# Performance work log

Hardware: AMD Instinct MI355X
Metric: run time of the kernel (lower is better)

## Reference

```python
import jax, jax.numpy as jnp
import numpy as np

B, S_IMG, S_TXT, D, H, HD = 1, 4096, 512, 3072, 24, 128
EPS = 1e-5
SCALE = 1.0 / np.sqrt(HD)


def _linear(x, W, b=None):
    # torch nn.Linear: y = x @ W.T + b, W is [out, in]
    y = jnp.einsum('bsd,od->bso', x, W)
    return y if b is None else y + b


def _rmsnorm(x, w):
    # over last dim (head_dim), torch nn.RMSNorm with affine weight
    var = jnp.mean(jnp.square(x), axis=-1, keepdims=True)
    return x * jax.lax.rsqrt(var + EPS) * w


def _rope(x, cos, sin):
    # x: [B, S, H, D]; cos/sin: [S, D]; interleaved-pair rotation
    xr = x.reshape(*x.shape[:-1], HD // 2, 2)
    x_real, x_imag = xr[..., 0], xr[..., 1]
    x_rot = jnp.stack([-x_imag, x_real], axis=-1).reshape(x.shape)
    return x * cos[None, :, None, :] + x_rot * sin[None, :, None, :]


def setup_inputs() -> dict:
    key = jax.random.key(0)
    ks = jax.random.split(key, 24)
    s = 0.02
    inp = {
        'hidden_states': jax.random.normal(ks[0], (B, S_IMG, D), jnp.float32),
        'encoder_hidden_states': jax.random.normal(ks[1], (B, S_TXT, D), jnp.float32),
        'rope_cos': jax.random.uniform(ks[2], (S_IMG + S_TXT, HD), jnp.float32),
        'rope_sin': jax.random.uniform(ks[3], (S_IMG + S_TXT, HD), jnp.float32),
        # image-stream qkv (bias=False)
        'Wq': jax.random.normal(ks[4], (D, D), jnp.float32) * s,
        'Wk': jax.random.normal(ks[5], (D, D), jnp.float32) * s,
        'Wv': jax.random.normal(ks[6], (D, D), jnp.float32) * s,
        # text-stream qkv (bias=True)
        'Waq': jax.random.normal(ks[7], (D, D), jnp.float32) * s,
        'baq': jnp.zeros((D,), jnp.float32),
        'Wak': jax.random.normal(ks[8], (D, D), jnp.float32) * s,
        'bak': jnp.zeros((D,), jnp.float32),
        'Wav': jax.random.normal(ks[9], (D, D), jnp.float32) * s,
        'bav': jnp.zeros((D,), jnp.float32),
        # output projections (bias=True)
        'Wo': jax.random.normal(ks[10], (D, D), jnp.float32) * s,
        'bo': jnp.zeros((D,), jnp.float32),
        'Wao': jax.random.normal(ks[11], (D, D), jnp.float32) * s,
        'bao': jnp.zeros((D,), jnp.float32),
        # RMSNorm weights on head_dim
        'wq_norm': jnp.ones((HD,), jnp.float32),
        'wk_norm': jnp.ones((HD,), jnp.float32),
        'waq_norm': jnp.ones((HD,), jnp.float32),
        'wak_norm': jnp.ones((HD,), jnp.float32),
    }
    return inp


def reference(hidden_states, encoder_hidden_states, rope_cos, rope_sin,
              Wq, Wk, Wv, Waq, baq, Wak, bak, Wav, bav,
              Wo, bo, Wao, bao, wq_norm, wk_norm, waq_norm, wak_norm):
    # image-stream qkv -> [B, S_img, H, HD]
    q = _linear(hidden_states, Wq).reshape(B, S_IMG, H, HD)
    k = _linear(hidden_states, Wk).reshape(B, S_IMG, H, HD)
    v = _linear(hidden_states, Wv).reshape(B, S_IMG, H, HD)
    q = _rmsnorm(q, wq_norm)
    k = _rmsnorm(k, wk_norm)
    # text-stream qkv -> [B, S_txt, H, HD]
    eq = _linear(encoder_hidden_states, Waq, baq).reshape(B, S_TXT, H, HD)
    ek = _linear(encoder_hidden_states, Wak, bak).reshape(B, S_TXT, H, HD)
    ev = _linear(encoder_hidden_states, Wav, bav).reshape(B, S_TXT, H, HD)
    eq = _rmsnorm(eq, waq_norm)
    ek = _rmsnorm(ek, wak_norm)
    # concat [encoder, image] along sequence
    q = jnp.concatenate([eq, q], axis=1)  # [B, S_total, H, HD]
    k = jnp.concatenate([ek, k], axis=1)
    v = jnp.concatenate([ev, v], axis=1)
    # RoPE on joint sequence
    q = _rope(q, rope_cos, rope_sin)
    k = _rope(k, rope_cos, rope_sin)
    # SDPA over joint sequence
    scores = jnp.einsum('bqhd,bkhd->bhqk', q, k) * SCALE
    probs = jax.nn.softmax(scores, axis=-1)
    out = jnp.einsum('bhqk,bkhd->bqhd', probs, v)  # [B, S_total, H, HD]
    out = out.reshape(B, S_IMG + S_TXT, D)
    enc_out = _linear(out[:, :S_TXT], Wao, bao)
    img_out = _linear(out[:, S_TXT:], Wo, bo)
    return (img_out, enc_out)
```

## Files before the change

### kernel.cpp

```cpp
#include <hip/hip_runtime.h>

typedef __bf16 bf16_t;
typedef __bf16 bf16x8 __attribute__((ext_vector_type(8)));
typedef float  f32x4  __attribute__((ext_vector_type(4)));

#define S_IMG 4096
#define S_TXT 512
#define S_TOT 4608
#define DMODEL 3072
#define NH 24
#define HD 128

__device__ __forceinline__ void load_lds16(const void* g, void* l) {
  __builtin_amdgcn_global_load_lds(
      (const __attribute__((address_space(1))) void*)g,
      (__attribute__((address_space(3))) void*)l, 16, 0, 0);
}

#define BARRIER() do { asm volatile("" ::: "memory");                          \
                       __builtin_amdgcn_s_barrier();                           \
                       asm volatile("" ::: "memory"); } while (0)

__global__ __launch_bounds__(256) void f2b_kernel(const float* __restrict__ in,
                                                  bf16_t* __restrict__ out, int n) {
  int i = (blockIdx.x * 256 + threadIdx.x) * 4;
  if (i >= n) return;
  float4 v = *(const float4*)(in + i);
  union { bf16_t b[4]; uint2 u; } pk;
  pk.b[0] = (bf16_t)v.x; pk.b[1] = (bf16_t)v.y;
  pk.b[2] = (bf16_t)v.z; pk.b[3] = (bf16_t)v.w;
  *(uint2*)(out + i) = pk.u;
}

template <typename OT>
__global__ __launch_bounds__(512, 2) void gemm256(
    const bf16_t* __restrict__ A0, const bf16_t* __restrict__ B0,
    OT* __restrict__ C0, const float* __restrict__ bias0, int mt0,
    const bf16_t* __restrict__ A1, const bf16_t* __restrict__ B1,
    OT* __restrict__ C1, const float* __restrict__ bias1, int swzq)
{
  const int NT = DMODEL / 64;
  __shared__ bf16_t As[2][2][256 * 32];
  __shared__ bf16_t Bs[2][2][256 * 32];

  int bid = blockIdx.x;
  int t = (bid & 7) * swzq + (bid >> 3);
  int nb0 = mt0 * 12;
  const bf16_t* A; const bf16_t* B; OT* C; const float* bias;
  if (t < nb0) { A = A0; B = B0; C = C0; bias = bias0; }
  else { t -= nb0; A = A1; B = B1; C = C1; bias = bias1; }
  int bx = t % 12, by = t / 12;

  int tid = threadIdx.x;
  int lane = tid & 63, wid = tid >> 6;
  int l15 = lane & 15, lg = lane >> 4;
  int wm = wid >> 2, wn = wid & 3;

  const bf16_t* Ag = A + (size_t)by * 256 * DMODEL;
  const bf16_t* Bg = B + (size_t)bx * 256 * DMODEL;

  int ur0 = tid >> 2;
  int uc0 = (tid & 3) * 8;

  auto stage = [&](int ht) {
    int T = ht >> 2, sl = ht & 3, kh = sl >> 1;
    const bf16_t* G = (sl & 1) ? Bg : Ag;
    bf16_t* L = (sl & 1) ? &Bs[T & 1][kh][0] : &As[T & 1][kh][0];
    int kbase = T * 64 + kh * 32;
    #pragma unroll
    for (int j = 0; j < 2; j++) {
      int r = j * 128 + ur0;
      load_lds16(G + (size_t)r * DMODEL + kbase + uc0,
                 (char*)L + (size_t)(j * 512 + tid) * 16);
    }
  };

  f32x4 acc[8][4];
  f32x4 zero = {0.f, 0.f, 0.f, 0.f};
  #pragma unroll
  for (int m = 0; m < 8; m++)
    #pragma unroll
    for (int n = 0; n < 4; n++) acc[m][n] = zero;

  stage(0); stage(1); stage(2); stage(3); stage(4); stage(5);
  asm volatile("s_waitcnt vmcnt(8)" ::: "memory");
  BARRIER();

  for (int T = 0; T < NT; ++T) {
    int cur = T & 1;
    const bf16_t* A0s = &As[cur][0][0];
    const bf16_t* A1s = &As[cur][1][0];
    const bf16_t* B0s = &Bs[cur][0][0];
    const bf16_t* B1s = &Bs[cur][1][0];
    bf16x8 af[4], bfr[4];

    #pragma unroll
    for (int n = 0; n < 4; n++)
      bfr[n] = *(const bf16x8*)(B0s + (wn * 64 + n * 16 + l15) * 32 + lg * 8);
    #pragma unroll
    for (int m = 0; m < 4; m++)
      af[m] = *(const bf16x8*)(A0s + (wm * 128 + m * 16 + l15) * 32 + lg * 8);
    if (T + 1 < NT) stage(4 * T + 6);
    BARRIER();
    __builtin_amdgcn_s_setprio(1);
    #pragma unroll
    for (int m = 0; m < 4; m++)
      #pragma unroll
      for (int n = 0; n < 4; n++)
        acc[m][n] = __builtin_amdgcn_mfma_f32_16x16x32_bf16(af[m], bfr[n], acc[m][n], 0, 0, 0);
    __builtin_amdgcn_s_setprio(0);
    BARRIER();

    #pragma unroll
    for (int m = 0; m < 4; m++)
      af[m] = *(const bf16x8*)(A0s + (wm * 128 + 64 + m * 16 + l15) * 32 + lg * 8);
    if (T + 1 < NT) stage(4 * T + 7);
    BARRIER();
    __builtin_amdgcn_s_setprio(1);
    #pragma unroll
    for (int m = 0; m < 4; m++)
      #pragma unroll
      for (int n = 0; n < 4; n++)
        acc[4 + m][n] = __builtin_amdgcn_mfma_f32_16x16x32_bf16(af[m], bfr[n], acc[4 + m][n], 0, 0, 0);
    __builtin_amdgcn_s_setprio(0);
    if (T < NT - 1) asm volatile("s_waitcnt vmcnt(8)" ::: "memory");
    else            asm volatile("s_waitcnt vmcnt(0)" ::: "memory");
    BARRIER();

    #pragma unroll
    for (int n = 0; n < 4; n++)
      bfr[n] = *(const bf16x8*)(B1s + (wn * 64 + n * 16 + l15) * 32 + lg * 8);
    #pragma unroll
    for (int m = 0; m < 4; m++)
      af[m] = *(const bf16x8*)(A1s + (wm * 128 + m * 16 + l15) * 32 + lg * 8);
    if (T + 2 < NT) stage(4 * T + 8);
    BARRIER();
    __builtin_amdgcn_s_setprio(1);
    #pragma unroll
    for (int m = 0; m < 4; m++)
      #pragma unroll
      for (int n = 0; n < 4; n++)
        acc[m][n] = __builtin_amdgcn_mfma_f32_16x16x32_bf16(af[m], bfr[n], acc[m][n], 0, 0, 0);
    __builtin_amdgcn_s_setprio(0);
    BARRIER();

    #pragma unroll
    for (int m = 0; m < 4; m++)
      af[m] = *(const bf16x8*)(A1s + (wm * 128 + 64 + m * 16 + l15) * 32 + lg * 8);
    if (T + 2 < NT) stage(4 * T + 9);
    BARRIER();
    __builtin_amdgcn_s_setprio(1);
    #pragma unroll
    for (int m = 0; m < 4; m++)
      #pragma unroll
      for (int n = 0; n < 4; n++)
        acc[4 + m][n] = __builtin_amdgcn_mfma_f32_16x16x32_bf16(af[m], bfr[n], acc[4 + m][n], 0, 0, 0);
    __builtin_amdgcn_s_setprio(0);
    if (T < NT - 2)      asm volatile("s_waitcnt vmcnt(8)" ::: "memory");
    else if (T == NT - 2) asm volatile("s_waitcnt vmcnt(4)" ::: "memory");
    BARRIER();
  }

  size_t row0 = (size_t)by * 256 + wm * 128;
  int col0 = bx * 256 + wn * 64;
  #pragma unroll
  for (int n = 0; n < 4; n++) {
    int col = col0 + n * 16 + l15;
    float bv = bias ? bias[col] : 0.f;
    #pragma unroll
    for (int m = 0; m < 8; m++) {
      #pragma unroll
      for (int r = 0; r < 4; r++) {
        size_t row = row0 + m * 16 + lg * 4 + r;
        C[row * DMODEL + col] = (OT)(acc[m][n][r] + bv);
      }
    }
  }
}

__global__ __launch_bounds__(256) void qk_post(
    const bf16_t* __restrict__ qbuf, const bf16_t* __restrict__ kbuf,
    const float* __restrict__ cosb, const float* __restrict__ sinb,
    const float* __restrict__ wqn, const float* __restrict__ wkn,
    const float* __restrict__ waqn, const float* __restrict__ wakn,
    bf16_t* __restrict__ Qh, bf16_t* __restrict__ Kh)
{
  int gw = blockIdx.x * 4 + (threadIdx.x >> 6);
  int lane = threadIdx.x & 63;
  int s = gw / NH, h = gw - (gw / NH) * NH;
  if (s >= S_TOT) return;
  int d0 = lane * 2;
  const bf16_t* qp = qbuf + (size_t)s * DMODEL + h * HD + d0;
  const bf16_t* kp = kbuf + (size_t)s * DMODEL + h * HD + d0;
  float q0 = (float)qp[0], q1 = (float)qp[1];
  float k0 = (float)kp[0], k1 = (float)kp[1];
  float sq = q0 * q0 + q1 * q1, sk = k0 * k0 + k1 * k1;
  #pragma unroll
  for (int m = 1; m < 64; m <<= 1) { sq += __shfl_xor(sq, m); sk += __shfl_xor(sk, m); }
  float rq = rsqrtf(sq * (1.f / HD) + 1e-5f);
  float rk = rsqrtf(sk * (1.f / HD) + 1e-5f);
  const float* qn = (s < S_TXT) ? waqn : wqn;
  const float* kn = (s < S_TXT) ? wakn : wkn;
  q0 *= rq * qn[d0]; q1 *= rq * qn[d0 + 1];
  k0 *= rk * kn[d0]; k1 *= rk * kn[d0 + 1];
  float c0 = cosb[s * HD + d0], c1 = cosb[s * HD + d0 + 1];
  float s0 = sinb[s * HD + d0], s1 = sinb[s * HD + d0 + 1];
  const float SCALE = 0.1275174319942397f;
  float oq0 = (q0 * c0 - q1 * s0) * SCALE;
  float oq1 = (q1 * c1 + q0 * s1) * SCALE;
  float ok0 = k0 * c0 - k1 * s0;
  float ok1 = k1 * c1 + k0 * s1;
  size_t ob = ((size_t)h * S_TOT + s) * HD + d0;
  union { bf16_t b[2]; unsigned int u; } pq, pk;
  pq.b[0] = (bf16_t)oq0; pq.b[1] = (bf16_t)oq1;
  pk.b[0] = (bf16_t)ok0; pk.b[1] = (bf16_t)ok1;
  *(unsigned int*)(Qh + ob) = pq.u;
  *(unsigned int*)(Kh + ob) = pk.u;
}

__global__ __launch_bounds__(256) void v_trans(const bf16_t* __restrict__ vbuf,
                                               bf16_t* __restrict__ Vt) {
  __shared__ bf16_t tile[64 * 130];
  int h = blockIdx.y, s0 = blockIdx.x * 64;
  int tid = threadIdx.x;
  #pragma unroll
  for (int i = 0; i < 16; i++) {
    int idx = tid + i * 256;
    int sr = idx >> 6, dp = idx & 63;
    unsigned int u = *(const unsigned int*)(vbuf + (size_t)(s0 + sr) * DMODEL + h * HD + dp * 2);
    *(unsigned int*)&tile[sr * 130 + dp * 2] = u;
  }
  __syncthreads();
  #pragma unroll
  for (int i = 0; i < 16; i++) {
    int idx = tid + i * 256;
    int d = idx >> 5, scp = idx & 31;
    union { bf16_t b[2]; unsigned int u; } pk;
    pk.b[0] = tile[(scp * 2) * 130 + d];
    pk.b[1] = tile[(scp * 2 + 1) * 130 + d];
    *(unsigned int*)(Vt + ((size_t)h * HD + d) * S_TOT + s0 + scp * 2) = pk.u;
  }
}

__global__ __launch_bounds__(256, 2) void attn_kernel(
    const bf16_t* __restrict__ Qh, const bf16_t* __restrict__ Kh,
    const bf16_t* __restrict__ Vt, bf16_t* __restrict__ O)
{
  int bid = blockIdx.x;
  int orig = (bid & 7) * 108 + (bid >> 3);
  int h = orig / 36;
  int q0 = (orig % 36) * 128;

  int tid = threadIdx.x, w = tid >> 6, lane = tid & 63;
  int l15 = lane & 15, lg = lane >> 4;
  int sw = (l15 & 7) << 4;

  __shared__ bf16_t Ks[2][64 * 128];
  __shared__ bf16_t Vs[2][128 * 64];
  __shared__ bf16_t Ps[4][32 * 64];

  const bf16_t* Kbase = Kh + (size_t)h * S_TOT * HD;
  const bf16_t* Vbase = Vt + (size_t)h * HD * S_TOT;
  bf16_t* Pw = &Ps[w][0];

  bf16x8 qf[2][4];
  #pragma unroll
  for (int qh = 0; qh < 2; qh++) {
    const bf16_t* Qrow = Qh + ((size_t)h * S_TOT + q0 + w * 32 + qh * 16 + l15) * HD + lg * 8;
    #pragma unroll
    for (int dc = 0; dc < 4; dc++) qf[qh][dc] = *(const bf16x8*)(Qrow + dc * 32);
  }

  f32x4 o[2][8];
  f32x4 zero = {0.f, 0.f, 0.f, 0.f};
  #pragma unroll
  for (int qh = 0; qh < 2; qh++)
    #pragma unroll
    for (int i = 0; i < 8; i++) o[qh][i] = zero;
  float m0 = -1e30f, m1 = -1e30f, l0 = 0.f, l1 = 0.f;

#define STAGE(buf, kt) do {                                                    \
    _Pragma("unroll")                                                          \
    for (int i_ = 0; i_ < 4; i_++) {                                           \
      int Lb = (tid + i_ * 256) * 16; int row = Lb >> 8, cb = Lb & 255;        \
      int sb = cb ^ ((row & 7) << 4);                                          \
      load_lds16(Kbase + (size_t)((kt) + row) * HD + (sb >> 1),                \
                 (char*)Ks[buf] + Lb);                                         \
    }                                                                          \
    _Pragma("unroll")                                                          \
    for (int i_ = 0; i_ < 4; i_++) {                                           \
      int Lb = (tid + i_ * 256) * 16; int row = Lb >> 7, cb = Lb & 127;        \
      int sb = cb ^ ((row & 7) << 4);                                          \
      load_lds16(Vbase + (size_t)row * S_TOT + (kt) + (sb >> 1),               \
                 (char*)Vs[buf] + Lb);                                         \
    }                                                                          \
  } while (0)

  STAGE(0, 0);
  __syncthreads();

  const int NT = S_TOT / 64;
  for (int t = 0; t < NT; ++t) {
    int cur = t & 1;
    if (t + 1 < NT) STAGE(cur ^ 1, (t + 1) * 64);

    f32x4 sacc[2][4];
    #pragma unroll
    for (int qh = 0; qh < 2; qh++)
      #pragma unroll
      for (int c = 0; c < 4; c++) sacc[qh][c] = zero;
    const char* Kc = (const char*)Ks[cur];
    #pragma unroll
    for (int c = 0; c < 4; c++) {
      int row = c * 16 + l15;
      int rs = (row & 7) << 4;
      const char* kr = Kc + row * 256;
      #pragma unroll
      for (int dc = 0; dc < 4; dc++) {
        bf16x8 kf = *(const bf16x8*)(kr + ((dc * 64 + lg * 16) ^ rs));
        sacc[0][c] = __builtin_amdgcn_mfma_f32_16x16x32_bf16(kf, qf[0][dc], sacc[0][c], 0, 0, 0);
        sacc[1][c] = __builtin_amdgcn_mfma_f32_16x16x32_bf16(kf, qf[1][dc], sacc[1][c], 0, 0, 0);
      }
    }

    float px0 = sacc[0][0][0], px1 = sacc[1][0][0];
    #pragma unroll
    for (int c = 0; c < 4; c++)
      #pragma unroll
      for (int r = 0; r < 4; r++) {
        px0 = fmaxf(px0, sacc[0][c][r]);
        px1 = fmaxf(px1, sacc[1][c][r]);
      }
    px0 = fmaxf(px0, __shfl_xor(px0, 16)); px0 = fmaxf(px0, __shfl_xor(px0, 32));
    px1 = fmaxf(px1, __shfl_xor(px1, 16)); px1 = fmaxf(px1, __shfl_xor(px1, 32));

    bool need = (px0 > m0 + 8.f) || (px1 > m1 + 8.f);
    if (__any(need)) {
      float mn0 = fmaxf(m0, px0), mn1 = fmaxf(m1, px1);
      float a0 = exp2f(m0 - mn0), a1 = exp2f(m1 - mn1);
      m0 = mn0; m1 = mn1; l0 *= a0; l1 *= a1;
      #pragma unroll
      for (int r = 0; r < 4; r++) {
        float f0 = __shfl(a0, lg * 4 + r);
        float f1 = __shfl(a1, lg * 4 + r);
        #pragma unroll
        for (int dn = 0; dn < 8; dn++) { o[0][dn][r] *= f0; o[1][dn][r] *= f1; }
      }
    }

    #pragma unroll
    for (int qh = 0; qh < 2; qh++) {
      float m = qh ? m1 : m0;
      float rsum = 0.f;
      char* Prow = (char*)Pw + (qh * 16 + l15) * 128;
      #pragma unroll
      for (int c = 0; c < 4; c++) {
        union { bf16_t b[4]; uint2 u; } pk;
        #pragma unroll
        for (int r = 0; r < 4; r++) {
          float p = exp2f(sacc[qh][c][r] - m);
          rsum += p;
          pk.b[r] = (bf16_t)p;
        }
        *(uint2*)(Prow + ((c * 32 + lg * 8) ^ sw)) = pk.u;
      }
      rsum += __shfl_xor(rsum, 16);
      rsum += __shfl_xor(rsum, 32);
      if (qh) l1 += rsum; else l0 += rsum;
    }

    bf16x8 pf[2][2];
    #pragma unroll
    for (int qh = 0; qh < 2; qh++) {
      const char* Prow = (const char*)Pw + (qh * 16 + l15) * 128;
      #pragma unroll
      for (int kc = 0; kc < 2; kc++)
        pf[qh][kc] = *(const bf16x8*)(Prow + ((kc * 64 + lg * 16) ^ sw));
    }
    const char* Vc = (const char*)Vs[cur];
    #pragma unroll
    for (int dn = 0; dn < 8; dn++) {
      int row = dn * 16 + l15;
      int rs2 = (row & 7) << 4;
      const char* vr = Vc + row * 128;
      bf16x8 vf0 = *(const bf16x8*)(vr + ((lg * 16) ^ rs2));
      bf16x8 vf1 = *(const bf16x8*)(vr + ((64 + lg * 16) ^ rs2));
      o[0][dn] = __builtin_amdgcn_mfma_f32_16x16x32_bf16(pf[0][0], vf0, o[0][dn], 0, 0, 0);
      o[0][dn] = __builtin_amdgcn_mfma_f32_16x16x32_bf16(pf[0][1], vf1, o[0][dn], 0, 0, 0);
      o[1][dn] = __builtin_amdgcn_mfma_f32_16x16x32_bf16(pf[1][0], vf0, o[1][dn], 0, 0, 0);
      o[1][dn] = __builtin_amdgcn_mfma_f32_16x16x32_bf16(pf[1][1], vf1, o[1][dn], 0, 0, 0);
    }

    __syncthreads();
  }
#undef STAGE

  #pragma unroll
  for (int qh = 0; qh < 2; qh++) {
    #pragma unroll
    for (int r = 0; r < 4; r++) {
      float lv = __shfl(qh ? l1 : l0, lg * 4 + r);
      float inv = 1.f / lv;
      size_t srow = (size_t)q0 + w * 32 + qh * 16 + lg * 4 + r;
      #pragma unroll
      for (int dn = 0; dn < 8; dn++)
        O[srow * DMODEL + h * HD + dn * 16 + l15] = (bf16_t)(o[qh][dn][r] * inv);
    }
  }
}

extern "C" void kernel_launch(void* const* d_in, const int* in_sizes, int n_in,
                              void* d_out, int out_size, void* d_ws, size_t ws_size,
                              hipStream_t stream) {
  const float* hidden = (const float*)d_in[0];
  const float* enc    = (const float*)d_in[1];
  const float* ropec  = (const float*)d_in[2];
  const float* ropes  = (const float*)d_in[3];
  const float* Wq  = (const float*)d_in[4];
  const float* Wk  = (const float*)d_in[5];
  const float* Wv  = (const float*)d_in[6];
  const float* Waq = (const float*)d_in[7];
  const float* baq = (const float*)d_in[8];
  const float* Wak = (const float*)d_in[9];
  const float* bak = (const float*)d_in[10];
  const float* Wav = (const float*)d_in[11];
  const float* bav = (const float*)d_in[12];
  const float* Wo  = (const float*)d_in[13];
  const float* bo  = (const float*)d_in[14];
  const float* Wao = (const float*)d_in[15];
  const float* bao = (const float*)d_in[16];
  const float* wqn = (const float*)d_in[17];
  const float* wkn = (const float*)d_in[18];
  const float* waqn = (const float*)d_in[19];
  const float* wakn = (const float*)d_in[20];

  const size_t WSZ = (size_t)DMODEL * DMODEL;
  const size_t SEQSZ = (size_t)S_TOT * DMODEL;
  if (ws_size < (2 * WSZ + 6 * SEQSZ) * sizeof(bf16_t)) return;

  bf16_t* s0   = (bf16_t*)d_ws;
  bf16_t* s1   = s0 + WSZ;
  bf16_t* xbi  = s1 + WSZ;
  bf16_t* xbt  = xbi + (size_t)S_IMG * DMODEL;
  bf16_t* qbuf = xbi + SEQSZ;
  bf16_t* kbuf = qbuf + SEQSZ;
  bf16_t* vbuf = kbuf + SEQSZ;
  bf16_t* Kh   = vbuf + SEQSZ;
  bf16_t* Vh   = Kh + SEQSZ;
  bf16_t* Qh   = xbi;
  bf16_t* attn_o = qbuf;
  float* outf = (float*)d_out;

  f2b_kernel<<<S_IMG * DMODEL / 1024, 256, 0, stream>>>(hidden, xbi, S_IMG * DMODEL);
  f2b_kernel<<<S_TXT * DMODEL / 1024, 256, 0, stream>>>(enc, xbt, S_TXT * DMODEL);

  const int WB = (int)(WSZ / 1024);
  f2b_kernel<<<WB, 256, 0, stream>>>(Wq,  s0, (int)WSZ);
  f2b_kernel<<<WB, 256, 0, stream>>>(Waq, s1, (int)WSZ);
  gemm256<bf16_t><<<216, 512, 0, stream>>>(
      xbi, s0, qbuf + (size_t)S_TXT * DMODEL, nullptr, 16,
      xbt, s1, qbuf, baq, 27);
  f2b_kernel<<<WB, 256, 0, stream>>>(Wk,  s0, (int)WSZ);
  f2b_kernel<<<WB, 256, 0, stream>>>(Wak, s1, (int)WSZ);
  gemm256<bf16_t><<<216, 512, 0, stream>>>(
      xbi, s0, kbuf + (size_t)S_TXT * DMODEL, nullptr, 16,
      xbt, s1, kbuf, bak, 27);
  f2b_kernel<<<WB, 256, 0, stream>>>(Wv,  s0, (int)WSZ);
  f2b_kernel<<<WB, 256, 0, stream>>>(Wav, s1, (int)WSZ);
  gemm256<bf16_t><<<216, 512, 0, stream>>>(
      xbi, s0, vbuf + (size_t)S_TXT * DMODEL, nullptr, 16,
      xbt, s1, vbuf, bav, 27);

  qk_post<<<S_TOT * NH / 4, 256, 0, stream>>>(qbuf, kbuf, ropec, ropes,
                                              wqn, wkn, waqn, wakn, Qh, Kh);
  v_trans<<<dim3(S_TOT / 64, NH), 256, 0, stream>>>(vbuf, Vh);

  attn_kernel<<<36 * 24, 256, 0, stream>>>(Qh, Kh, Vh, attn_o);

  f2b_kernel<<<WB, 256, 0, stream>>>(Wo,  s0, (int)WSZ);
  f2b_kernel<<<WB, 256, 0, stream>>>(Wao, s1, (int)WSZ);
  gemm256<float><<<216, 512, 0, stream>>>(
      attn_o + (size_t)S_TXT * DMODEL, s0, outf, bo, 16,
      attn_o, s1, outf + (size_t)S_IMG * DMODEL, bao, 27);
}
```

Before: 1.007 ms.

## Swizzle GEMM LDS reads and shrink attention KV tile to 32 for occupancy

After: 1.357 ms. 1.35x slower.

```diff
diff --git a/kernel.cpp b/kernel.cpp
--- a/kernel.cpp
+++ b/kernel.cpp
@@ -55,12 +55,13 @@
   int lane = tid & 63, wid = tid >> 6;
   int l15 = lane & 15, lg = lane >> 4;
   int wm = wid >> 2, wn = wid & 3;
+  int sx = (lg ^ ((l15 >> 1) & 3)) * 8;
 
   const bf16_t* Ag = A + (size_t)by * 256 * DMODEL;
   const bf16_t* Bg = B + (size_t)bx * 256 * DMODEL;
 
   int ur0 = tid >> 2;
-  int uc0 = (tid & 3) * 8;
+  int uc0 = ((tid & 3) ^ ((tid >> 3) & 3)) * 8;
 
   auto stage = [&](int ht) {
     int T = ht >> 2, sl = ht & 3, kh = sl >> 1;
@@ -96,10 +97,10 @@
 
     #pragma unroll
     for (int n = 0; n < 4; n++)
-      bfr[n] = *(const bf16x8*)(B0s + (wn * 64 + n * 16 + l15) * 32 + lg * 8);
-    #pragma unroll
-    for (int m = 0; m < 4; m++)
-      af[m] = *(const bf16x8*)(A0s + (wm * 128 + m * 16 + l15) * 32 + lg * 8);
+      bfr[n] = *(const bf16x8*)(B0s + (wn * 64 + n * 16 + l15) * 32 + sx);
+    #pragma unroll
+    for (int m = 0; m < 4; m++)
+      af[m] = *(const bf16x8*)(A0s + (wm * 128 + m * 16 + l15) * 32 + sx);
     if (T + 1 < NT) stage(4 * T + 6);
     BARRIER();
     __builtin_amdgcn_s_setprio(1);
@@ -113,7 +114,7 @@
 
     #pragma unroll
     for (int m = 0; m < 4; m++)
-      af[m] = *(const bf16x8*)(A0s + (wm * 128 + 64 + m * 16 + l15) * 32 + lg * 8);
+      af[m] = *(const bf16x8*)(A0s + (wm * 128 + 64 + m * 16 + l15) * 32 + sx);
     if (T + 1 < NT) stage(4 * T + 7);
     BARRIER();
     __builtin_amdgcn_s_setprio(1);
@@ -129,10 +130,10 @@
 
     #pragma unroll
     for (int n = 0; n < 4; n++)
-      bfr[n] = *(const bf16x8*)(B1s + (wn * 64 + n * 16 + l15) * 32 + lg * 8);
-    #pragma unroll
-    for (int m = 0; m < 4; m++)
-      af[m] = *(const bf16x8*)(A1s + (wm * 128 + m * 16 + l15) * 32 + lg * 8);
+      bfr[n] = *(const bf16x8*)(B1s + (wn * 64 + n * 16 + l15) * 32 + sx);
+    #pragma unroll
+    for (int m = 0; m < 4; m++)
+      af[m] = *(const bf16x8*)(A1s + (wm * 128 + m * 16 + l15) * 32 + sx);
     if (T + 2 < NT) stage(4 * T + 8);
     BARRIER();
     __builtin_amdgcn_s_setprio(1);
@@ -146,7 +147,7 @@
 
     #pragma unroll
     for (int m = 0; m < 4; m++)
-      af[m] = *(const bf16x8*)(A1s + (wm * 128 + 64 + m * 16 + l15) * 32 + lg * 8);
+      af[m] = *(const bf16x8*)(A1s + (wm * 128 + 64 + m * 16 + l15) * 32 + sx);
     if (T + 2 < NT) stage(4 * T + 9);
     BARRIER();
     __builtin_amdgcn_s_setprio(1);
@@ -156,7 +157,7 @@
       for (int n = 0; n < 4; n++)
         acc[4 + m][n] = __builtin_amdgcn_mfma_f32_16x16x32_bf16(af[m], bfr[n], acc[4 + m][n], 0, 0, 0);
     __builtin_amdgcn_s_setprio(0);
-    if (T < NT - 2)      asm volatile("s_waitcnt vmcnt(8)" ::: "memory");
+    if (T < NT - 2)       asm volatile("s_waitcnt vmcnt(8)" ::: "memory");
     else if (T == NT - 2) asm volatile("s_waitcnt vmcnt(4)" ::: "memory");
     BARRIER();
   }
@@ -242,7 +243,7 @@
   }
 }
 
-__global__ __launch_bounds__(256, 2) void attn_kernel(
+__global__ __launch_bounds__(256, 4) void attn_kernel(
     const bf16_t* __restrict__ Qh, const bf16_t* __restrict__ Kh,
     const bf16_t* __restrict__ Vt, bf16_t* __restrict__ O)
 {
@@ -253,11 +254,11 @@
 
   int tid = threadIdx.x, w = tid >> 6, lane = tid & 63;
   int l15 = lane & 15, lg = lane >> 4;
-  int sw = (l15 & 7) << 4;
-
-  __shared__ bf16_t Ks[2][64 * 128];
-  __shared__ bf16_t Vs[2][128 * 64];
-  __shared__ bf16_t Ps[4][32 * 64];
+  int s3 = (l15 >> 1) & 3;
+
+  __shared__ bf16_t Ks[2][32 * 128];
+  __shared__ bf16_t Vs[2][128 * 32];
+  __shared__ bf16_t Ps[4][32 * 32];
 
   const bf16_t* Kbase = Kh + (size_t)h * S_TOT * HD;
   const bf16_t* Vbase = Vt + (size_t)h * HD * S_TOT;
@@ -281,16 +282,16 @@
 
 #define STAGE(buf, kt) do {                                                    \
     _Pragma("unroll")                                                          \
-    for (int i_ = 0; i_ < 4; i_++) {                                           \
+    for (int i_ = 0; i_ < 2; i_++) {                    \
       int Lb = (tid + i_ * 256) * 16; int row = Lb >> 8, cb = Lb & 255;        \
       int sb = cb ^ ((row & 7) << 4);                                          \
       load_lds16(Kbase + (size_t)((kt) + row) * HD + (sb >> 1),                \
                  (char*)Ks[buf] + Lb);                                         \
     }                                                                          \
     _Pragma("unroll")                                                          \
-    for (int i_ = 0; i_ < 4; i_++) {                                           \
-      int Lb = (tid + i_ * 256) * 16; int row = Lb >> 7, cb = Lb & 127;        \
-      int sb = cb ^ ((row & 7) << 4);                                          \
+    for (int i_ = 0; i_ < 2; i_++) {                    \
+      int Lb = (tid + i_ * 256) * 16; int row = Lb >> 6, cb = Lb & 63;         \
+      int sb = cb ^ (((row >> 1) & 3) << 4);                                   \
       load_lds16(Vbase + (size_t)row * S_TOT + (kt) + (sb >> 1),               \
                  (char*)Vs[buf] + Lb);                                         \
     }                                                                          \
@@ -299,19 +300,19 @@
   STAGE(0, 0);
   __syncthreads();
 
-  const int NT = S_TOT / 64;
+  const int NT = S_TOT / 32;
   for (int t = 0; t < NT; ++t) {
     int cur = t & 1;
-    if (t + 1 < NT) STAGE(cur ^ 1, (t + 1) * 64);
-
-    f32x4 sacc[2][4];
+    if (t + 1 < NT) STAGE(cur ^ 1, (t + 1) * 32);
+
+    f32x4 sacc[2][2];
     #pragma unroll
     for (int qh = 0; qh < 2; qh++)
       #pragma unroll
-      for (int c = 0; c < 4; c++) sacc[qh][c] = zero;
+      for (int c = 0; c < 2; c++) sacc[qh][c] = zero;
     const char* Kc = (const char*)Ks[cur];
     #pragma unroll
-    for (int c = 0; c < 4; c++) {
+    for (int c = 0; c < 2; c++) {
       int row = c * 16 + l15;
       int rs = (row & 7) << 4;
       const char* kr = Kc + row * 256;
@@ -325,7 +326,7 @@
 
     float px0 = sacc[0][0][0], px1 = sacc[1][0][0];
     #pragma unroll
-    for (int c = 0; c < 4; c++)
+    for (int c = 0; c < 2; c++)
       #pragma unroll
       for (int r = 0; r < 4; r++) {
         px0 = fmaxf(px0, sacc[0][c][r]);
@@ -352,9 +353,9 @@
     for (int qh = 0; qh < 2; qh++) {
       float m = qh ? m1 : m0;
       float rsum = 0.f;
-      char* Prow = (char*)Pw + (qh * 16 + l15) * 128;
-      #pragma unroll
-      for (int c = 0; c < 4; c++) {
+      char* Prow = (char*)Pw + (qh * 16 + l15) * 64;
+      #pragma unroll
+      for (int c = 0; c < 2; c++) {
         union { bf16_t b[4]; uint2 u; } pk;
         #pragma unroll
         for (int r = 0; r < 4; r++) {
@@ -362,33 +363,26 @@
           rsum += p;
           pk.b[r] = (bf16_t)p;
         }
-        *(uint2*)(Prow + ((c * 32 + lg * 8) ^ sw)) = pk.u;
+        *(uint2*)(Prow + (((c * 4 + lg) ^ (s3 << 1)) * 8)) = pk.u;
       }
       rsum += __shfl_xor(rsum, 16);
       rsum += __shfl_xor(rsum, 32);
       if (qh) l1 += rsum; else l0 += rsum;
     }
 
-    bf16x8 pf[2][2];
-    #pragma unroll
-    for (int qh = 0; qh < 2; qh++) {
-      const char* Prow = (const char*)Pw + (qh * 16 + l15) * 128;
-      #pragma unroll
-      for (int kc = 0; kc < 2; kc++)
-        pf[qh][kc] = *(const bf16x8*)(Prow + ((kc * 64 + lg * 16) ^ sw));
-    }
+    bf16x8 pf[2];
+    #pragma unroll
+    for (int qh = 0; qh < 2; qh++)
+      pf[qh] = *(const bf16x8*)((const char*)Pw + (qh * 16 + l15) * 64 +
+                                ((lg ^ s3) * 16));
     const char* Vc = (const char*)Vs[cur];
+    int vsw = (lg * 16) ^ (s3 << 4);
     #pragma unroll
     for (int dn = 0; dn < 8; dn++) {
       int row = dn * 16 + l15;
-      int rs2 = (row & 7) << 4;
-      const char* vr = Vc + row * 128;
-      bf16x8 vf0 = *(const bf16x8*)(vr + ((lg * 16) ^ rs2));
-      bf16x8 vf1 = *(const bf16x8*)(vr + ((64 + lg * 16) ^ rs2));
-      o[0][dn] = __builtin_amdgcn_mfma_f32_16x16x32_bf16(pf[0][0], vf0, o[0][dn], 0, 0, 0);
-      o[0][dn] = __builtin_amdgcn_mfma_f32_16x16x32_bf16(pf[0][1], vf1, o[0][dn], 0, 0, 0);
-      o[1][dn] = __builtin_amdgcn_mfma_f32_16x16x32_bf16(pf[1][0], vf0, o[1][dn], 0, 0, 0);
-      o[1][dn] = __builtin_amdgcn_mfma_f32_16x16x32_bf16(pf[1][1], vf1, o[1][dn], 0, 0, 0);
+      bf16x8 vf = *(const bf16x8*)(Vc + row * 64 + vsw);
+      o[0][dn] = __builtin_amdgcn_mfma_f32_16x16x32_bf16(pf[0], vf, o[0][dn], 0, 0, 0);
+      o[1][dn] = __builtin_amdgcn_mfma_f32_16x16x32_bf16(pf[1], vf, o[1][dn], 0, 0, 0);
     }
 
     __syncthreads();
```
